# Kernel tuning notes

Measured on AMD Instinct MI355X. Metric: run time of the kernel, lower is better.

Reference implementation:

```python
import jax, jax.numpy as jnp
import numpy as np

COORD = 5.0
NOOBJ = 0.5


def _reflat(x):
    # torch: flatten(x.transpose(0,1), start_dim=1).transpose(0,1) -> [B*S*S, C]
    C = x.shape[1]
    return jnp.moveaxis(x, 1, -1).reshape(-1, C)


def setup_inputs() -> dict:
    key = jax.random.key(0)
    k1, k2 = jax.random.split(key)
    B, C, S = 256, 25, 64
    inp = jax.random.uniform(k1, (B, C, S, S), dtype=jnp.float32)
    tgt = jax.random.uniform(k2, (B, C, S, S), dtype=jnp.float32)
    return {"input": inp, "target": tgt}


def _iou(b1, b2, blocks):
    # vectorized, detached IoU between predicted and target boxes, per row
    b1 = jax.lax.stop_gradient(b1)
    b2 = jax.lax.stop_gradient(b2)
    c1 = b1[:, :2] / blocks
    c2 = b2[:, :2] / blocks
    x1a, x2a = c1[:, 0] - b1[:, 2] / 2, c1[:, 0] + b1[:, 2] / 2
    y1a, y2a = c1[:, 1] - b1[:, 3] / 2, c1[:, 1] + b1[:, 3] / 2
    x1b, x2b = c2[:, 0] - b2[:, 2] / 2, c2[:, 0] + b2[:, 2] / 2
    y1b, y2b = c2[:, 1] - b2[:, 3] / 2, c2[:, 1] + b2[:, 3] / 2
    dx = jnp.minimum(x2a, x2b) - jnp.maximum(x1a, x1b)
    dy = jnp.minimum(y2a, y2b) - jnp.maximum(y1a, y1b)
    inter = dx * dy
    union = b1[:, 2] * b1[:, 3] + b2[:, 2] * b2[:, 3] - inter
    pos = (dx > 0) & (dy > 0)
    return jnp.where(pos, inter / jnp.where(pos, union, 1.0), 0.0)


def reference(input, target):
    blocks = target.shape[-1]
    t = _reflat(target)  # [N, C]
    p = _reflat(input)   # [N, C]
    m = (t[:, 4] > 0).astype(p.dtype)  # responsible-cell mask [N]
    iou = _iou(p[:, :4], t[:, :4], blocks)  # detached target confidence
    sp = jnp.sqrt(p[:, 2:4])
    st = jnp.sqrt(t[:, 2:4])
    m2 = m[:, None]
    loss = COORD * jnp.sum(m2 * jnp.square(p[:, :2] - t[:, :2]))
    loss += COORD * jnp.sum(m2 * jnp.square(sp - st))
    loss += jnp.sum(m * jnp.square(p[:, 4] - iou))
    loss += NOOBJ * jnp.sum((1.0 - m) * jnp.square(p[:, 4]))
    loss += jnp.sum(m2 * jnp.square(p[:, 5:] - t[:, 5:]))
    return loss
```

## Files before the change

### kernel.cpp

```cpp
#include <hip/hip_runtime.h>


#define COORD 5.0f
#define NOOBJ 0.5f

constexpr int B = 256;
constexpr int C = 25;
constexpr int S = 64;
constexpr int SS = S * S;
constexpr int CH_STRIDE4 = SS / 4;
constexpr int IMG_STRIDE4 = C * CH_STRIDE4;
constexpr int N4 = B * SS / 4;

constexpr int THREADS = 256;
constexpr int CLASS_CH = 20;
constexpr int CLASS_ITEMS = CLASS_CH * N4;
constexpr int CLASS_BLOCKS = 2560;
constexpr int CLASS_THREADS_TOT = CLASS_BLOCKS * THREADS;
constexpr int CLASS_IPT = CLASS_ITEMS / CLASS_THREADS_TOT;
constexpr int BOX_BLOCKS = N4 / THREADS;
constexpr int TOTAL_BLOCKS = CLASS_BLOCKS + BOX_BLOCKS;
constexpr int MASK_BYTES = N4 * 4;

__device__ __forceinline__ float comp(const float4 v, int k) {
    switch (k) {
        case 0: return v.x;
        case 1: return v.y;
        case 2: return v.z;
        default: return v.w;
    }
}

__global__ void zero_out_kernel(float* out) { out[0] = 0.0f; }

__global__ __launch_bounds__(256) void mask_kernel(
        const float4* __restrict__ tg, uchar4* __restrict__ mask) {
    const int g = blockIdx.x * 256 + threadIdx.x;
    const float4 t4 = tg[(g >> 10) * IMG_STRIDE4 + (g & 1023) + 4 * CH_STRIDE4];
    mask[g] = make_uchar4(t4.x > 0.0f, t4.y > 0.0f, t4.z > 0.0f, t4.w > 0.0f);
}

__global__ __launch_bounds__(256, 4) void yolo_loss_kernel(
        const float4* __restrict__ in, const float4* __restrict__ tg,
        const uchar4* __restrict__ mask,
        float* __restrict__ out) {
    float acc = 0.0f;

    if (blockIdx.x < CLASS_BLOCKS) {
        const int t = blockIdx.x * THREADS + threadIdx.x;
        #pragma unroll
        for (int i = 0; i < CLASS_IPT; i += 4) {
            float4 pv[4], tv[4];
            uchar4 mk[4];
            #pragma unroll
            for (int u = 0; u < 4; ++u) {
                const int itm = t + (i + u) * CLASS_THREADS_TOT;
                const int c = 5 + (itm >> 18);
                const int g = itm & (N4 - 1);
                const int base = (g >> 10) * IMG_STRIDE4 + (g & 1023);
                pv[u] = in[base + c * CH_STRIDE4];
                tv[u] = tg[base + c * CH_STRIDE4];
                if (mask) {
                    mk[u] = mask[g];
                } else {
                    const float4 t4 = tg[base + 4 * CH_STRIDE4];
                    mk[u] = make_uchar4(t4.x > 0.0f, t4.y > 0.0f,
                                        t4.z > 0.0f, t4.w > 0.0f);
                }
            }
            #pragma unroll
            for (int u = 0; u < 4; ++u) {
                float d;
                d = pv[u].x - tv[u].x; if (mk[u].x) acc += d * d;
                d = pv[u].y - tv[u].y; if (mk[u].y) acc += d * d;
                d = pv[u].z - tv[u].z; if (mk[u].z) acc += d * d;
                d = pv[u].w - tv[u].w; if (mk[u].w) acc += d * d;
            }
        }
    } else {
        const int g = (blockIdx.x - CLASS_BLOCKS) * THREADS + threadIdx.x;
        const int base = (g >> 10) * IMG_STRIDE4 + (g & 1023);

        const float4 p0 = in[base + 0 * CH_STRIDE4];
        const float4 p1 = in[base + 1 * CH_STRIDE4];
        const float4 p2 = in[base + 2 * CH_STRIDE4];
        const float4 p3 = in[base + 3 * CH_STRIDE4];
        const float4 p4 = in[base + 4 * CH_STRIDE4];
        const float4 t0 = tg[base + 0 * CH_STRIDE4];
        const float4 t1 = tg[base + 1 * CH_STRIDE4];
        const float4 t2 = tg[base + 2 * CH_STRIDE4];
        const float4 t3 = tg[base + 3 * CH_STRIDE4];
        const float4 t4 = tg[base + 4 * CH_STRIDE4];

        const float invBlocks = 1.0f / (float)S;
        #pragma unroll
        for (int k = 0; k < 4; ++k) {
            const float px = comp(p0, k), py = comp(p1, k);
            const float pw = comp(p2, k), ph = comp(p3, k);
            const float pc = comp(p4, k);
            const float tx = comp(t0, k), ty = comp(t1, k);
            const float tw = comp(t2, k), th = comp(t3, k);
            const float tc = comp(t4, k);
            const float m = (tc > 0.0f) ? 1.0f : 0.0f;

            const float c1x = px * invBlocks, c1y = py * invBlocks;
            const float c2x = tx * invBlocks, c2y = ty * invBlocks;
            const float x1a = c1x - pw * 0.5f, x2a = c1x + pw * 0.5f;
            const float y1a = c1y - ph * 0.5f, y2a = c1y + ph * 0.5f;
            const float x1b = c2x - tw * 0.5f, x2b = c2x + tw * 0.5f;
            const float y1b = c2y - th * 0.5f, y2b = c2y + th * 0.5f;
            const float dx = fminf(x2a, x2b) - fmaxf(x1a, x1b);
            const float dy = fminf(y2a, y2b) - fmaxf(y1a, y1b);
            const float inter = dx * dy;
            const float uni = pw * ph + tw * th - inter;
            const bool pos = (dx > 0.0f) && (dy > 0.0f);
            const float iou = pos ? (inter / uni) : 0.0f;

            const float ex = px - tx, ey = py - ty;
            acc += COORD * m * (ex * ex + ey * ey);
            const float sw = sqrtf(pw) - sqrtf(tw);
            const float sh = sqrtf(ph) - sqrtf(th);
            acc += COORD * m * (sw * sw + sh * sh);
            const float ec = pc - iou;
            acc += m * ec * ec;
            acc += NOOBJ * (1.0f - m) * (pc * pc);
        }
    }

    #pragma unroll
    for (int off = 32; off > 0; off >>= 1)
        acc += __shfl_down(acc, off, 64);

    __shared__ float smem[4];
    const int lane = threadIdx.x & 63;
    const int wid = threadIdx.x >> 6;
    if (lane == 0) smem[wid] = acc;
    __syncthreads();
    if (threadIdx.x == 0) {
        const float s = smem[0] + smem[1] + smem[2] + smem[3];
        atomicAdd(out, s);
    }
}

extern "C" void kernel_launch(void* const* d_in, const int* in_sizes, int n_in,
                              void* d_out, int out_size, void* d_ws, size_t ws_size,
                              hipStream_t stream) {
    const float4* in = (const float4*)d_in[0];
    const float4* tg = (const float4*)d_in[1];
    float* out = (float*)d_out;

    zero_out_kernel<<<1, 1, 0, stream>>>(out);

    uchar4* mask = nullptr;
    if (d_ws != nullptr && ws_size >= (size_t)MASK_BYTES) {
        mask = (uchar4*)d_ws;
        mask_kernel<<<N4 / 256, 256, 0, stream>>>(tg, mask);
    }

    yolo_loss_kernel<<<TOTAL_BLOCKS, THREADS, 0, stream>>>(in, tg, mask, out);
}
```

Before: 230.1 us.

## Split fused loss kernel into class and box kernels with float mask

Breaks the single branchy kernel into a class-channel kernel and a separate box kernel, each launched on its own. The mask is stored as float4 (1.0/0.0) instead of uchar4 so the class loop can use branch-free FMA accumulation. Class blocks drop from 2560 to 2048 and the unroll changes from 4 to 2. The float mask quadruples the mask traffic (16 bytes per 4 cells instead of 4) and adds one more kernel launch, in exchange for simpler control flow and lower register pressure.

```diff
diff --git a/kernel.cpp b/kernel.cpp
--- a/kernel.cpp
+++ b/kernel.cpp
@@ -15,12 +15,11 @@
 constexpr int THREADS = 256;
 constexpr int CLASS_CH = 20;
 constexpr int CLASS_ITEMS = CLASS_CH * N4;
-constexpr int CLASS_BLOCKS = 2560;
+constexpr int CLASS_BLOCKS = 2048;
 constexpr int CLASS_THREADS_TOT = CLASS_BLOCKS * THREADS;
 constexpr int CLASS_IPT = CLASS_ITEMS / CLASS_THREADS_TOT;
 constexpr int BOX_BLOCKS = N4 / THREADS;
-constexpr int TOTAL_BLOCKS = CLASS_BLOCKS + BOX_BLOCKS;
-constexpr int MASK_BYTES = N4 * 4;
+constexpr int MASK_BYTES = N4 * 16;
 
 __device__ __forceinline__ float comp(const float4 v, int k) {
     switch (k) {
@@ -31,115 +30,134 @@
     }
 }
 
-__global__ void zero_out_kernel(float* out) { out[0] = 0.0f; }
-
-__global__ __launch_bounds__(256) void mask_kernel(
-        const float4* __restrict__ tg, uchar4* __restrict__ mask) {
-    const int g = blockIdx.x * 256 + threadIdx.x;
-    const float4 t4 = tg[(g >> 10) * IMG_STRIDE4 + (g & 1023) + 4 * CH_STRIDE4];
-    mask[g] = make_uchar4(t4.x > 0.0f, t4.y > 0.0f, t4.z > 0.0f, t4.w > 0.0f);
-}
-
-__global__ __launch_bounds__(256, 4) void yolo_loss_kernel(
-        const float4* __restrict__ in, const float4* __restrict__ tg,
-        const uchar4* __restrict__ mask,
-        float* __restrict__ out) {
-    float acc = 0.0f;
-
-    if (blockIdx.x < CLASS_BLOCKS) {
-        const int t = blockIdx.x * THREADS + threadIdx.x;
-        #pragma unroll
-        for (int i = 0; i < CLASS_IPT; i += 4) {
-            float4 pv[4], tv[4];
-            uchar4 mk[4];
-            #pragma unroll
-            for (int u = 0; u < 4; ++u) {
-                const int itm = t + (i + u) * CLASS_THREADS_TOT;
-                const int c = 5 + (itm >> 18);
-                const int g = itm & (N4 - 1);
-                const int base = (g >> 10) * IMG_STRIDE4 + (g & 1023);
-                pv[u] = in[base + c * CH_STRIDE4];
-                tv[u] = tg[base + c * CH_STRIDE4];
-                if (mask) {
-                    mk[u] = mask[g];
-                } else {
-                    const float4 t4 = tg[base + 4 * CH_STRIDE4];
-                    mk[u] = make_uchar4(t4.x > 0.0f, t4.y > 0.0f,
-                                        t4.z > 0.0f, t4.w > 0.0f);
-                }
-            }
-            #pragma unroll
-            for (int u = 0; u < 4; ++u) {
-                float d;
-                d = pv[u].x - tv[u].x; if (mk[u].x) acc += d * d;
-                d = pv[u].y - tv[u].y; if (mk[u].y) acc += d * d;
-                d = pv[u].z - tv[u].z; if (mk[u].z) acc += d * d;
-                d = pv[u].w - tv[u].w; if (mk[u].w) acc += d * d;
-            }
-        }
-    } else {
-        const int g = (blockIdx.x - CLASS_BLOCKS) * THREADS + threadIdx.x;
-        const int base = (g >> 10) * IMG_STRIDE4 + (g & 1023);
-
-        const float4 p0 = in[base + 0 * CH_STRIDE4];
-        const float4 p1 = in[base + 1 * CH_STRIDE4];
-        const float4 p2 = in[base + 2 * CH_STRIDE4];
-        const float4 p3 = in[base + 3 * CH_STRIDE4];
-        const float4 p4 = in[base + 4 * CH_STRIDE4];
-        const float4 t0 = tg[base + 0 * CH_STRIDE4];
-        const float4 t1 = tg[base + 1 * CH_STRIDE4];
-        const float4 t2 = tg[base + 2 * CH_STRIDE4];
-        const float4 t3 = tg[base + 3 * CH_STRIDE4];
-        const float4 t4 = tg[base + 4 * CH_STRIDE4];
-
-        const float invBlocks = 1.0f / (float)S;
-        #pragma unroll
-        for (int k = 0; k < 4; ++k) {
-            const float px = comp(p0, k), py = comp(p1, k);
-            const float pw = comp(p2, k), ph = comp(p3, k);
-            const float pc = comp(p4, k);
-            const float tx = comp(t0, k), ty = comp(t1, k);
-            const float tw = comp(t2, k), th = comp(t3, k);
-            const float tc = comp(t4, k);
-            const float m = (tc > 0.0f) ? 1.0f : 0.0f;
-
-            const float c1x = px * invBlocks, c1y = py * invBlocks;
-            const float c2x = tx * invBlocks, c2y = ty * invBlocks;
-            const float x1a = c1x - pw * 0.5f, x2a = c1x + pw * 0.5f;
-            const float y1a = c1y - ph * 0.5f, y2a = c1y + ph * 0.5f;
-            const float x1b = c2x - tw * 0.5f, x2b = c2x + tw * 0.5f;
-            const float y1b = c2y - th * 0.5f, y2b = c2y + th * 0.5f;
-            const float dx = fminf(x2a, x2b) - fmaxf(x1a, x1b);
-            const float dy = fminf(y2a, y2b) - fmaxf(y1a, y1b);
-            const float inter = dx * dy;
-            const float uni = pw * ph + tw * th - inter;
-            const bool pos = (dx > 0.0f) && (dy > 0.0f);
-            const float iou = pos ? (inter / uni) : 0.0f;
-
-            const float ex = px - tx, ey = py - ty;
-            acc += COORD * m * (ex * ex + ey * ey);
-            const float sw = sqrtf(pw) - sqrtf(tw);
-            const float sh = sqrtf(ph) - sqrtf(th);
-            acc += COORD * m * (sw * sw + sh * sh);
-            const float ec = pc - iou;
-            acc += m * ec * ec;
-            acc += NOOBJ * (1.0f - m) * (pc * pc);
-        }
-    }
-
+__device__ __forceinline__ void block_reduce_atomic(float acc, float* out) {
     #pragma unroll
     for (int off = 32; off > 0; off >>= 1)
         acc += __shfl_down(acc, off, 64);
-
     __shared__ float smem[4];
     const int lane = threadIdx.x & 63;
     const int wid = threadIdx.x >> 6;
     if (lane == 0) smem[wid] = acc;
     __syncthreads();
     if (threadIdx.x == 0) {
-        const float s = smem[0] + smem[1] + smem[2] + smem[3];
-        atomicAdd(out, s);
+        atomicAdd(out, smem[0] + smem[1] + smem[2] + smem[3]);
     }
+}
+
+__global__ void zero_out_kernel(float* out) { out[0] = 0.0f; }
+
+__global__ __launch_bounds__(256) void mask_kernel(
+        const float4* __restrict__ tg, float4* __restrict__ mask) {
+    const int g = blockIdx.x * 256 + threadIdx.x;
+    const float4 t4 = tg[(g >> 10) * IMG_STRIDE4 + (g & 1023) + 4 * CH_STRIDE4];
+    mask[g] = make_float4(t4.x > 0.0f ? 1.0f : 0.0f,
+                          t4.y > 0.0f ? 1.0f : 0.0f,
+                          t4.z > 0.0f ? 1.0f : 0.0f,
+                          t4.w > 0.0f ? 1.0f : 0.0f);
+}
+
+__global__ __launch_bounds__(256) void class_kernel(
+        const float4* __restrict__ in, const float4* __restrict__ tg,
+        const float4* __restrict__ mask,
+        float* __restrict__ out) {
+    const int t = blockIdx.x * THREADS + threadIdx.x;
+    float acc = 0.0f;
+
+    #pragma unroll
+    for (int i = 0; i < CLASS_IPT; i += 2) {
+        const int f0 = t + (i + 0) * CLASS_THREADS_TOT;
+        const int f1 = t + (i + 1) * CLASS_THREADS_TOT;
+        const int c0 = 5 + (f0 >> 18);
+        const int c1 = 5 + (f1 >> 18);
+        const int g0 = f0 & (N4 - 1);
+        const int g1 = f1 & (N4 - 1);
+        const int b0 = (g0 >> 10) * IMG_STRIDE4 + (g0 & 1023);
+        const int b1 = (g1 >> 10) * IMG_STRIDE4 + (g1 & 1023);
+
+        const float4 pv0 = in[b0 + c0 * CH_STRIDE4];
+        const float4 tv0 = tg[b0 + c0 * CH_STRIDE4];
+        const float4 pv1 = in[b1 + c1 * CH_STRIDE4];
+        const float4 tv1 = tg[b1 + c1 * CH_STRIDE4];
+        float4 m0, m1;
+        if (mask) {
+            m0 = mask[g0];
+            m1 = mask[g1];
+        } else {
+            const float4 a = tg[b0 + 4 * CH_STRIDE4];
+            const float4 b = tg[b1 + 4 * CH_STRIDE4];
+            m0 = make_float4(a.x > 0.0f ? 1.0f : 0.0f, a.y > 0.0f ? 1.0f : 0.0f,
+                             a.z > 0.0f ? 1.0f : 0.0f, a.w > 0.0f ? 1.0f : 0.0f);
+            m1 = make_float4(b.x > 0.0f ? 1.0f : 0.0f, b.y > 0.0f ? 1.0f : 0.0f,
+                             b.z > 0.0f ? 1.0f : 0.0f, b.w > 0.0f ? 1.0f : 0.0f);
+        }
+
+        float d;
+        d = pv0.x - tv0.x; acc = fmaf(m0.x * d, d, acc);
+        d = pv0.y - tv0.y; acc = fmaf(m0.y * d, d, acc);
+        d = pv0.z - tv0.z; acc = fmaf(m0.z * d, d, acc);
+        d = pv0.w - tv0.w; acc = fmaf(m0.w * d, d, acc);
+        d = pv1.x - tv1.x; acc = fmaf(m1.x * d, d, acc);
+        d = pv1.y - tv1.y; acc = fmaf(m1.y * d, d, acc);
+        d = pv1.z - tv1.z; acc = fmaf(m1.z * d, d, acc);
+        d = pv1.w - tv1.w; acc = fmaf(m1.w * d, d, acc);
+    }
+
+    block_reduce_atomic(acc, out);
+}
+
+__global__ __launch_bounds__(256) void box_kernel(
+        const float4* __restrict__ in, const float4* __restrict__ tg,
+        float* __restrict__ out) {
+    const int g = blockIdx.x * THREADS + threadIdx.x;
+    const int base = (g >> 10) * IMG_STRIDE4 + (g & 1023);
+
+    const float4 p0 = in[base + 0 * CH_STRIDE4];
+    const float4 p1 = in[base + 1 * CH_STRIDE4];
+    const float4 p2 = in[base + 2 * CH_STRIDE4];
+    const float4 p3 = in[base + 3 * CH_STRIDE4];
+    const float4 p4 = in[base + 4 * CH_STRIDE4];
+    const float4 t0 = tg[base + 0 * CH_STRIDE4];
+    const float4 t1 = tg[base + 1 * CH_STRIDE4];
+    const float4 t2 = tg[base + 2 * CH_STRIDE4];
+    const float4 t3 = tg[base + 3 * CH_STRIDE4];
+    const float4 t4 = tg[base + 4 * CH_STRIDE4];
+
+    float acc = 0.0f;
+    const float invBlocks = 1.0f / (float)S;
+    #pragma unroll
+    for (int k = 0; k < 4; ++k) {
+        const float px = comp(p0, k), py = comp(p1, k);
+        const float pw = comp(p2, k), ph = comp(p3, k);
+        const float pc = comp(p4, k);
+        const float tx = comp(t0, k), ty = comp(t1, k);
+        const float tw = comp(t2, k), th = comp(t3, k);
+        const float tc = comp(t4, k);
+        const float m = (tc > 0.0f) ? 1.0f : 0.0f;
+
+        const float c1x = px * invBlocks, c1y = py * invBlocks;
+        const float c2x = tx * invBlocks, c2y = ty * invBlocks;
+        const float x1a = c1x - pw * 0.5f, x2a = c1x + pw * 0.5f;
+        const float y1a = c1y - ph * 0.5f, y2a = c1y + ph * 0.5f;
+        const float x1b = c2x - tw * 0.5f, x2b = c2x + tw * 0.5f;
+        const float y1b = c2y - th * 0.5f, y2b = c2y + th * 0.5f;
+        const float dx = fminf(x2a, x2b) - fmaxf(x1a, x1b);
+        const float dy = fminf(y2a, y2b) - fmaxf(y1a, y1b);
+        const float inter = dx * dy;
+        const float uni = pw * ph + tw * th - inter;
+        const bool pos = (dx > 0.0f) && (dy > 0.0f);
+        const float iou = pos ? (inter / uni) : 0.0f;
+
+        const float ex = px - tx, ey = py - ty;
+        acc += COORD * m * (ex * ex + ey * ey);
+        const float sw = sqrtf(pw) - sqrtf(tw);
+        const float sh = sqrtf(ph) - sqrtf(th);
+        acc += COORD * m * (sw * sw + sh * sh);
+        const float ec = pc - iou;
+        acc += m * ec * ec;
+        acc += NOOBJ * (1.0f - m) * (pc * pc);
+    }
+
+    block_reduce_atomic(acc, out);
 }
 
 extern "C" void kernel_launch(void* const* d_in, const int* in_sizes, int n_in,
@@ -151,11 +169,12 @@
 
     zero_out_kernel<<<1, 1, 0, stream>>>(out);
 
-    uchar4* mask = nullptr;
+    float4* mask = nullptr;
     if (d_ws != nullptr && ws_size >= (size_t)MASK_BYTES) {
-        mask = (uchar4*)d_ws;
+        mask = (float4*)d_ws;
         mask_kernel<<<N4 / 256, 256, 0, stream>>>(tg, mask);
     }
 
-    yolo_loss_kernel<<<TOTAL_BLOCKS, THREADS, 0, stream>>>(in, tg, mask, out);
+    class_kernel<<<CLASS_BLOCKS, THREADS, 0, stream>>>(in, tg, mask, out);
+    box_kernel<<<BOX_BLOCKS, THREADS, 0, stream>>>(in, tg, out);
 }
```

Measured after the change: 233.2 us. Within noise of the previous version (+1.3%).
